# Performance work log

Hardware: AMD Instinct MI355X
Metric: run time of the kernel (lower is better)

The kernel has to match this reference:

```python
import jax, jax.numpy as jnp
import numpy as np

ALPHA = 2.0


def _masked_logsumexp(S):
    # log-sum-exp over axis 1 with the diagonal excluded (j != i)
    n = S.shape[0]
    Sm = jnp.where(jnp.eye(n, dtype=bool), -jnp.inf, S)
    return jax.nn.logsumexp(Sm, axis=1)


def setup_inputs() -> dict:
    key = jax.random.key(0)
    k1, k2, k3 = jax.random.split(key, 3)
    n, d = 8192, 128
    scale = 0.1  # keep exp(dot) in a reasonable range
    z_au = jax.random.normal(k1, (n, d), dtype=jnp.float32) * scale
    z_tp = jax.random.normal(k2, (n, d), dtype=jnp.float32) * scale
    fc_weights = jax.random.normal(k3, (2, d), dtype=jnp.float32) * scale
    return {"z_au": z_au, "z_tp": z_tp, "fc_weights": fc_weights}


def reference(z_au, z_tp, fc_weights):
    n, d = z_au.shape
    nf = jnp.float32(n)

    # pairwise dot-product similarities (cosim is a plain dot in the original)
    S_aa = z_au @ z_au.T          # [n, n]
    S_tt = z_tp @ z_tp.T          # [n, n]
    S_at = z_au @ z_tp.T          # [n, n]

    # pos_loss[i] = log(sum_{j!=i} exp(S_aa[i,j]) + exp(S_tt[i,j]))
    # implemented as a single stable logsumexp over concatenated columns
    eye = jnp.eye(n, dtype=bool)
    S_pos = jnp.concatenate(
        [jnp.where(eye, -jnp.inf, S_aa), jnp.where(eye, -jnp.inf, S_tt)], axis=1
    )  # [n, 2n]
    pos = jax.nn.logsumexp(S_pos, axis=1)  # [n]

    # neg_loss[i] = log(sum_{j!=i} exp(S_at[i,j]))
    neg = _masked_logsumexp(S_at)  # [n]

    # alpha * cosim(z_au[i], z_tp[i])
    diag_at = jnp.diagonal(S_at)  # [n]

    # supcon_loss in the original is an [n, d] tensor filled with the scalar
    # sum_i (-pos_i + neg_i + alpha * diag_i); track the scalar, account for
    # the final torch.sum over [n, d] with a factor n*d.
    supcon = jnp.sum(-pos + neg + ALPHA * diag_at)

    # pt_loss: sum_i [-<z_au_i, pt0> + <z_au_i, pt1> - <z_tp_i, pt1> + <z_tp_i, pt0>] / n
    pt0, pt1 = fc_weights[0], fc_weights[1]
    pt_loss = (
        jnp.dot(jnp.sum(z_au, axis=0), pt1 - pt0)
        + jnp.dot(jnp.sum(z_tp, axis=0), pt0 - pt1)
    ) / nf

    # esupcon_loss = 1/(n+2) * (pt_loss + supcon_loss) broadcast to [n, d];
    # torch.sum over that tensor -> multiply scalar by n*d
    return (nf * jnp.float32(d)) / (nf + 2.0) * (pt_loss + supcon)
```

## Files before the change

### kernel.cpp

```cpp
#include <hip/hip_runtime.h>

typedef __attribute__((ext_vector_type(8))) short bf16x8;
typedef __attribute__((ext_vector_type(4))) float f32x4;
typedef unsigned int u32;
typedef unsigned short u16;

#define NROWS 8192
#define NDIM 128
#define NSPLIT 16
#define COLS_PER_SPLIT (NROWS / NSPLIT)
#define BN 64
#define ITERS (COLS_PER_SPLIT / BN)

#define SQRT_LOG2E 1.2011224087864498f
#define TWO_OVER_LOG2E 1.3862943611198906f

__device__ __forceinline__ float hw_exp2(float x) {
  float r;
  asm("v_exp_f32 %0, %1" : "=v"(r) : "v"(x));
  return r;
}


__device__ __forceinline__ u16 f2bf(float x) {
  u32 u = __float_as_uint(x);
  u32 r = (u + 0x7fffu + ((u >> 16) & 1u)) >> 16;
  return (u16)r;
}

__global__ __launch_bounds__(256) void esupcon_convert(
    const float* __restrict__ za, const float* __restrict__ zt,
    const float* __restrict__ w, u16* __restrict__ zabf,
    u16* __restrict__ ztbf, float* __restrict__ pt_part) {
  const int b = blockIdx.x, t = threadIdx.x;
  const bool tp = b >= 1024;
  const float* src = tp ? zt : za;
  u16* dst = tp ? ztbf : zabf;
  const int base = ((b & 1023) * 256 + t) * 4;
  float4 v = *reinterpret_cast<const float4*>(src + base);

  const int k = base & (NDIM - 1);
  float p = v.x * (w[NDIM + k + 0] - w[k + 0]) + v.y * (w[NDIM + k + 1] - w[k + 1]) +
            v.z * (w[NDIM + k + 2] - w[k + 2]) + v.w * (w[NDIM + k + 3] - w[k + 3]);
  if (tp) p = -p;

  ushort4 o;
  o.x = f2bf(v.x * SQRT_LOG2E);
  o.y = f2bf(v.y * SQRT_LOG2E);
  o.z = f2bf(v.z * SQRT_LOG2E);
  o.w = f2bf(v.w * SQRT_LOG2E);
  *reinterpret_cast<ushort4*>(dst + base) = o;

  __shared__ float red[256];
  red[t] = p;
  __syncthreads();
  for (int st = 128; st > 0; st >>= 1) {
    if (t < st) red[t] += red[t + st];
    __syncthreads();
  }
  if (t == 0) pt_part[b] = red[0];
}


template <bool MASK>
__device__ __forceinline__ void epilogue(const f32x4 (&acc)[3][2][2],
                                         float (&poss)[2][4], float (&negs)[2][4],
                                         float* __restrict__ diagv, int wrow0,
                                         int colw0, int lane) {
#pragma unroll
  for (int rt = 0; rt < 2; ++rt)
#pragma unroll
    for (int ct = 0; ct < 2; ++ct) {
      const int col_g = colw0 + ct * 16 + (lane & 15);
      const int rbase = wrow0 + rt * 16 + ((lane >> 4) << 2);
#pragma unroll
      for (int r = 0; r < 4; ++r) {
        float eaa = hw_exp2(acc[0][rt][ct][r]);
        float ett = hw_exp2(acc[1][rt][ct][r]);
        float vat = acc[2][rt][ct][r];
        float eat = hw_exp2(vat);
        float ppos = eaa + ett;
        if (MASK) {
          const bool dia = (rbase + r) == col_g;
          if (dia) {
            diagv[rbase + r] = vat;
            ppos = 0.f;
            eat = 0.f;
          }
        }
        poss[rt][r] += ppos;
        negs[rt][r] += eat;
      }
    }
}

__global__ __launch_bounds__(256, 2) void esupcon_stage1(
    const u16* __restrict__ zabf, const u16* __restrict__ ztbf,
    float* __restrict__ pos_part, float* __restrict__ neg_part,
    float* __restrict__ diagv) {
  __shared__ __align__(16) char lds[2][32768];

  const int tid = threadIdx.x;
  const int lane = tid & 63;
  const int wid = tid >> 6;
  const int wr = wid >> 1, wc = wid & 1;
  const int by = blockIdx.x;
  const int bx = blockIdx.y;
  const int wrow0 = by * 64 + wr * 32;

  bf16x8 afrag[2][2][4];
  {
    const int rlo = lane & 15, kg = lane >> 4;
#pragma unroll
    for (int rt = 0; rt < 2; ++rt) {
      const u16* pa = zabf + (size_t)(wrow0 + rt * 16 + rlo) * NDIM + kg * 8;
      const u16* pt = ztbf + (size_t)(wrow0 + rt * 16 + rlo) * NDIM + kg * 8;
#pragma unroll
      for (int s = 0; s < 4; ++s) {
        afrag[0][rt][s] = *reinterpret_cast<const bf16x8*>(pa + s * 32);
        afrag[1][rt][s] = *reinterpret_cast<const bf16x8*>(pt + s * 32);
      }
    }
  }

  float poss[2][4], negs[2][4];
#pragma unroll
  for (int rt = 0; rt < 2; ++rt)
#pragma unroll
    for (int r = 0; r < 4; ++r) {
      poss[rt][r] = 0.f;
      negs[rt][r] = 0.f;
    }

  auto stage = [&](int buf, int it) {
    const int col0g = bx * COLS_PER_SPLIT + it * BN;
    const char* gA = (const char*)(zabf + (size_t)col0g * NDIM);
    const char* gT = (const char*)(ztbf + (size_t)col0g * NDIM);
    char* lA = &lds[buf][0];
    char* lT = &lds[buf][16384];
#pragma unroll
    for (int i = 0; i < 4; ++i) {
      const int chunk = wid * 4 + i;
      const int y = chunk * 1024 + lane * 16;
      const int ysw = y ^ (((y >> 8) & 7) << 4);
      __builtin_amdgcn_global_load_lds(
          (const __attribute__((address_space(1))) u32*)(gA + ysw),
          (__attribute__((address_space(3))) u32*)(lA + chunk * 1024), 16, 0, 0);
      __builtin_amdgcn_global_load_lds(
          (const __attribute__((address_space(1))) u32*)(gT + ysw),
          (__attribute__((address_space(3))) u32*)(lT + chunk * 1024), 16, 0, 0);
    }
  };

  int cur = 0;
  stage(0, 0);

  for (int it = 0; it < ITERS; ++it) {
    asm volatile("s_waitcnt vmcnt(0)" ::: "memory");
    __builtin_amdgcn_s_barrier();
    asm volatile("" ::: "memory");

    if (it + 1 < ITERS) stage(cur ^ 1, it + 1);

    const char* lA = &lds[cur][0];
    const char* lT = &lds[cur][16384];

    f32x4 acc[3][2][2] = {};
#pragma unroll
    for (int s = 0; s < 4; ++s) {
      bf16x8 bA[2], bT[2];
#pragma unroll
      for (int ct = 0; ct < 2; ++ct) {
        const int c = wc * 32 + ct * 16 + (lane & 15);
        const int off = (c * 256 + s * 64 + (lane >> 4) * 16) ^ ((c & 7) << 4);
        bA[ct] = *reinterpret_cast<const bf16x8*>(lA + off);
        bT[ct] = *reinterpret_cast<const bf16x8*>(lT + off);
      }
#pragma unroll
      for (int rt = 0; rt < 2; ++rt)
#pragma unroll
        for (int ct = 0; ct < 2; ++ct) {
          acc[0][rt][ct] = __builtin_amdgcn_mfma_f32_16x16x32_bf16(
              afrag[0][rt][s], bA[ct], acc[0][rt][ct], 0, 0, 0);
          acc[1][rt][ct] = __builtin_amdgcn_mfma_f32_16x16x32_bf16(
              afrag[1][rt][s], bT[ct], acc[1][rt][ct], 0, 0, 0);
          acc[2][rt][ct] = __builtin_amdgcn_mfma_f32_16x16x32_bf16(
              afrag[0][rt][s], bT[ct], acc[2][rt][ct], 0, 0, 0);
        }
    }

    const int col0g = bx * COLS_PER_SPLIT + it * BN;
    const bool hasdiag = (col0g == by * 64);
    if (hasdiag)
      epilogue<true>(acc, poss, negs, diagv, wrow0, col0g + wc * 32, lane);
    else
      epilogue<false>(acc, poss, negs, diagv, wrow0, col0g + wc * 32, lane);

    cur ^= 1;
  }

#pragma unroll
  for (int m = 1; m < 16; m <<= 1) {
#pragma unroll
    for (int rt = 0; rt < 2; ++rt)
#pragma unroll
      for (int r = 0; r < 4; ++r) {
        poss[rt][r] += __shfl_xor(poss[rt][r], m, 64);
        negs[rt][r] += __shfl_xor(negs[rt][r], m, 64);
      }
  }

  if ((lane & 15) == 0) {
    const int sp = bx * 2 + wc;
#pragma unroll
    for (int rt = 0; rt < 2; ++rt) {
      const int rbase = wrow0 + rt * 16 + ((lane >> 4) << 2);
#pragma unroll
      for (int r = 0; r < 4; ++r) {
        pos_part[(size_t)(rbase + r) * 32 + sp] = poss[rt][r];
        neg_part[(size_t)(rbase + r) * 32 + sp] = negs[rt][r];
      }
    }
  }
}


__global__ __launch_bounds__(256) void esupcon_reduce1(
    const float* __restrict__ pos_part, const float* __restrict__ neg_part,
    const float* __restrict__ diagv, const float* __restrict__ pt_part,
    float* __restrict__ part_out ) {
  const int b = blockIdx.x, t = threadIdx.x;
  const int r = b * 256 + t;
  const f32x4* pp = reinterpret_cast<const f32x4*>(pos_part + (size_t)r * 32);
  const f32x4* np = reinterpret_cast<const f32x4*>(neg_part + (size_t)r * 32);
  float P = 0.f, Nn = 0.f;
#pragma unroll
  for (int s = 0; s < 8; ++s) {
    f32x4 a = pp[s], c = np[s];
    P += a[0] + a[1] + a[2] + a[3];
    Nn += c[0] + c[1] + c[2] + c[3];
  }
  float sc = -logf(P) + logf(Nn) + TWO_OVER_LOG2E * diagv[r];
  float pt = (t < 64) ? pt_part[b * 64 + t] : 0.f;

  __shared__ float s1[256], s2[256];
  s1[t] = sc;
  s2[t] = pt;
  __syncthreads();
  for (int st = 128; st > 0; st >>= 1) {
    if (t < st) {
      s1[t] += s1[t + st];
      s2[t] += s2[t + st];
    }
    __syncthreads();
  }
  if (t == 0) {
    part_out[b] = s1[0];
    part_out[32 + b] = s2[0];
  }
}


__global__ __launch_bounds__(64) void esupcon_reduce2(
    const float* __restrict__ part_out, float* __restrict__ out) {
  const int t = threadIdx.x;
  float sc = (t < 32) ? part_out[t] : 0.f;
  float pt = (t < 32) ? part_out[32 + t] : 0.f;
#pragma unroll
  for (int m = 1; m < 64; m <<= 1) {
    sc += __shfl_xor(sc, m, 64);
    pt += __shfl_xor(pt, m, 64);
  }
  if (t == 0) {
    const float pt_loss = pt / (float)NROWS;
    out[0] = ((float)NROWS * (float)NDIM / ((float)NROWS + 2.0f)) * (pt_loss + sc);
  }
}


extern "C" void kernel_launch(void* const* d_in, const int* in_sizes, int n_in,
                              void* d_out, int out_size, void* d_ws, size_t ws_size,
                              hipStream_t stream) {
  const float* za = (const float*)d_in[0];
  const float* zt = (const float*)d_in[1];
  const float* w = (const float*)d_in[2];
  float* out = (float*)d_out;

  char* ws = (char*)d_ws;
  u16* zabf = (u16*)ws;
  u16* ztbf = (u16*)(ws + (size_t)(1 << 21));
  float* pos_part = (float*)(ws + (size_t)(2 << 21));
  float* neg_part = (float*)(ws + (size_t)(2 << 21) + (1 << 20));
  float* diagv = (float*)(ws + (size_t)(2 << 21) + (2 << 20));
  float* pt_part = (float*)(ws + (size_t)(2 << 21) + (2 << 20) + (1 << 15));
  float* part_out = (float*)(ws + (size_t)(2 << 21) + (2 << 20) + (1 << 15) + (1 << 13));

  esupcon_convert<<<dim3(2048), dim3(256), 0, stream>>>(za, zt, w, zabf, ztbf, pt_part);
  esupcon_stage1<<<dim3(NROWS / 64, NSPLIT), dim3(256), 0, stream>>>(
      zabf, ztbf, pos_part, neg_part, diagv);
  esupcon_reduce1<<<dim3(32), dim3(256), 0, stream>>>(pos_part, neg_part, diagv,
                                                      pt_part, part_out);
  esupcon_reduce2<<<dim3(1), dim3(64), 0, stream>>>(part_out, out);
}
```

Measured before the change: 80.09 us.

## Restructure stage1 into single-wave blocks with 64-row A fragments and 16-column tiles

Each block becomes one 64-lane wavefront that keeps A and T fragments for 64 rows in registers and streams 16-column tiles of both matrices through double-buffered LDS. Waiting on vmcnt(8) after issuing the next tile's loads replaces the block-wide barrier, so the next prefetch overlaps the current tile's compute. The goal is to drop the cross-wave barrier and raise B-operand reuse per LDS load across four row tiles. In exchange, register pressure goes up and grid parallelism per block goes down. The partial layout shrinks to 16 strips per row, and reduce1 is updated to match.

```diff
diff --git a/kernel.cpp b/kernel.cpp
--- a/kernel.cpp
+++ b/kernel.cpp
@@ -7,10 +7,10 @@
 
 #define NROWS 8192
 #define NDIM 128
-#define NSPLIT 16
-#define COLS_PER_SPLIT (NROWS / NSPLIT)
-#define BN 64
-#define ITERS (COLS_PER_SPLIT / BN)
+#define NSTRIP 16
+#define COLS_PER_STRIP (NROWS / NSTRIP)
+#define BN 16
+#define WITERS (COLS_PER_STRIP / BN)
 
 #define SQRT_LOG2E 1.2011224087864498f
 #define TWO_OVER_LOG2E 1.3862943611198906f
@@ -63,146 +63,140 @@
 
 
 template <bool MASK>
-__device__ __forceinline__ void epilogue(const f32x4 (&acc)[3][2][2],
-                                         float (&poss)[2][4], float (&negs)[2][4],
-                                         float* __restrict__ diagv, int wrow0,
-                                         int colw0, int lane) {
-#pragma unroll
-  for (int rt = 0; rt < 2; ++rt)
-#pragma unroll
-    for (int ct = 0; ct < 2; ++ct) {
-      const int col_g = colw0 + ct * 16 + (lane & 15);
-      const int rbase = wrow0 + rt * 16 + ((lane >> 4) << 2);
-#pragma unroll
-      for (int r = 0; r < 4; ++r) {
-        float eaa = hw_exp2(acc[0][rt][ct][r]);
-        float ett = hw_exp2(acc[1][rt][ct][r]);
-        float vat = acc[2][rt][ct][r];
-        float eat = hw_exp2(vat);
-        float ppos = eaa + ett;
-        if (MASK) {
-          const bool dia = (rbase + r) == col_g;
-          if (dia) {
-            diagv[rbase + r] = vat;
-            ppos = 0.f;
-            eat = 0.f;
-          }
+__device__ __forceinline__ void compute_tile(
+    const char* __restrict__ lA, const char* __restrict__ lT,
+    const bf16x8 (&afA)[4][4], const bf16x8 (&afT)[4][4],
+    float (&poss)[4][4], float (&negs)[4][4], float* __restrict__ diagv,
+    int row0, int col0, int lane) {
+  const int lc = lane & 15, kg = lane >> 4;
+  const int colg = col0 + lc;
+
+  f32x4 accA[4] = {};
+#pragma unroll
+  for (int s = 0; s < 4; ++s) {
+    const int off = (lc * 256 + s * 64 + kg * 16) ^ ((lc & 7) << 4);
+    bf16x8 b = *reinterpret_cast<const bf16x8*>(lA + off);
+#pragma unroll
+    for (int rt = 0; rt < 4; ++rt)
+      accA[rt] = __builtin_amdgcn_mfma_f32_16x16x32_bf16(afA[rt][s], b, accA[rt], 0, 0, 0);
+  }
+#pragma unroll
+  for (int rt = 0; rt < 4; ++rt)
+#pragma unroll
+    for (int r = 0; r < 4; ++r) {
+      float e = hw_exp2(accA[rt][r]);
+      if (MASK && (row0 + rt * 16 + kg * 4 + r) == colg) e = 0.f;
+      poss[rt][r] += e;
+    }
+
+  f32x4 accT[4] = {}, accX[4] = {};
+#pragma unroll
+  for (int s = 0; s < 4; ++s) {
+    const int off = (lc * 256 + s * 64 + kg * 16) ^ ((lc & 7) << 4);
+    bf16x8 b = *reinterpret_cast<const bf16x8*>(lT + off);
+#pragma unroll
+    for (int rt = 0; rt < 4; ++rt) {
+      accT[rt] = __builtin_amdgcn_mfma_f32_16x16x32_bf16(afT[rt][s], b, accT[rt], 0, 0, 0);
+      accX[rt] = __builtin_amdgcn_mfma_f32_16x16x32_bf16(afA[rt][s], b, accX[rt], 0, 0, 0);
+    }
+  }
+#pragma unroll
+  for (int rt = 0; rt < 4; ++rt)
+#pragma unroll
+    for (int r = 0; r < 4; ++r) {
+      float ett = hw_exp2(accT[rt][r]);
+      float vat = accX[rt][r];
+      float eat = hw_exp2(vat);
+      if (MASK) {
+        const bool dia = (row0 + rt * 16 + kg * 4 + r) == colg;
+        if (dia) {
+          diagv[colg] = vat;
+          ett = 0.f;
+          eat = 0.f;
         }
-        poss[rt][r] += ppos;
-        negs[rt][r] += eat;
-      }
-    }
-}
-
-__global__ __launch_bounds__(256, 2) void esupcon_stage1(
+      }
+      poss[rt][r] += ett;
+      negs[rt][r] += eat;
+    }
+}
+
+__global__ __launch_bounds__(64, 2) void esupcon_stage1(
     const u16* __restrict__ zabf, const u16* __restrict__ ztbf,
     float* __restrict__ pos_part, float* __restrict__ neg_part,
     float* __restrict__ diagv) {
-  __shared__ __align__(16) char lds[2][32768];
-
-  const int tid = threadIdx.x;
-  const int lane = tid & 63;
-  const int wid = tid >> 6;
-  const int wr = wid >> 1, wc = wid & 1;
-  const int by = blockIdx.x;
-  const int bx = blockIdx.y;
-  const int wrow0 = by * 64 + wr * 32;
-
-  bf16x8 afrag[2][2][4];
+  __shared__ __align__(16) char lds[2][8192];
+
+  const int lane = threadIdx.x;
+  const int rg = blockIdx.x;
+  const int cs = blockIdx.y;
+  const int row0 = rg * 64;
+
+  bf16x8 afA[4][4], afT[4][4];
   {
     const int rlo = lane & 15, kg = lane >> 4;
 #pragma unroll
-    for (int rt = 0; rt < 2; ++rt) {
-      const u16* pa = zabf + (size_t)(wrow0 + rt * 16 + rlo) * NDIM + kg * 8;
-      const u16* pt = ztbf + (size_t)(wrow0 + rt * 16 + rlo) * NDIM + kg * 8;
+    for (int rt = 0; rt < 4; ++rt) {
+      const u16* pa = zabf + (size_t)(row0 + rt * 16 + rlo) * NDIM + kg * 8;
+      const u16* pt = ztbf + (size_t)(row0 + rt * 16 + rlo) * NDIM + kg * 8;
 #pragma unroll
       for (int s = 0; s < 4; ++s) {
-        afrag[0][rt][s] = *reinterpret_cast<const bf16x8*>(pa + s * 32);
-        afrag[1][rt][s] = *reinterpret_cast<const bf16x8*>(pt + s * 32);
-      }
-    }
-  }
-
-  float poss[2][4], negs[2][4];
-#pragma unroll
-  for (int rt = 0; rt < 2; ++rt)
-#pragma unroll
-    for (int r = 0; r < 4; ++r) {
-      poss[rt][r] = 0.f;
-      negs[rt][r] = 0.f;
-    }
+        afA[rt][s] = *reinterpret_cast<const bf16x8*>(pa + s * 32);
+        afT[rt][s] = *reinterpret_cast<const bf16x8*>(pt + s * 32);
+      }
+    }
+  }
+
+  float poss[4][4] = {}, negs[4][4] = {};
 
   auto stage = [&](int buf, int it) {
-    const int col0g = bx * COLS_PER_SPLIT + it * BN;
-    const char* gA = (const char*)(zabf + (size_t)col0g * NDIM);
-    const char* gT = (const char*)(ztbf + (size_t)col0g * NDIM);
-    char* lA = &lds[buf][0];
-    char* lT = &lds[buf][16384];
-#pragma unroll
-    for (int i = 0; i < 4; ++i) {
-      const int chunk = wid * 4 + i;
-      const int y = chunk * 1024 + lane * 16;
+    const size_t colbase = (size_t)(cs * COLS_PER_STRIP + it * BN) * NDIM;
+    const char* gA = (const char*)(zabf + colbase);
+    const char* gT = (const char*)(ztbf + colbase);
+    char* dst = &lds[buf][0];
+#pragma unroll
+    for (int j = 0; j < 4; ++j) {
+      const int y = j * 1024 + lane * 16;
       const int ysw = y ^ (((y >> 8) & 7) << 4);
       __builtin_amdgcn_global_load_lds(
           (const __attribute__((address_space(1))) u32*)(gA + ysw),
-          (__attribute__((address_space(3))) u32*)(lA + chunk * 1024), 16, 0, 0);
+          (__attribute__((address_space(3))) u32*)(dst + j * 1024), 16, 0, 0);
+    }
+#pragma unroll
+    for (int j = 0; j < 4; ++j) {
+      const int y = j * 1024 + lane * 16;
+      const int ysw = y ^ (((y >> 8) & 7) << 4);
       __builtin_amdgcn_global_load_lds(
           (const __attribute__((address_space(1))) u32*)(gT + ysw),
-          (__attribute__((address_space(3))) u32*)(lT + chunk * 1024), 16, 0, 0);
+          (__attribute__((address_space(3))) u32*)(dst + 4096 + j * 1024), 16, 0, 0);
     }
   };
 
+  stage(0, 0);
   int cur = 0;
-  stage(0, 0);
-
-  for (int it = 0; it < ITERS; ++it) {
-    asm volatile("s_waitcnt vmcnt(0)" ::: "memory");
-    __builtin_amdgcn_s_barrier();
-    asm volatile("" ::: "memory");
-
-    if (it + 1 < ITERS) stage(cur ^ 1, it + 1);
-
-    const char* lA = &lds[cur][0];
-    const char* lT = &lds[cur][16384];
-
-    f32x4 acc[3][2][2] = {};
-#pragma unroll
-    for (int s = 0; s < 4; ++s) {
-      bf16x8 bA[2], bT[2];
-#pragma unroll
-      for (int ct = 0; ct < 2; ++ct) {
-        const int c = wc * 32 + ct * 16 + (lane & 15);
-        const int off = (c * 256 + s * 64 + (lane >> 4) * 16) ^ ((c & 7) << 4);
-        bA[ct] = *reinterpret_cast<const bf16x8*>(lA + off);
-        bT[ct] = *reinterpret_cast<const bf16x8*>(lT + off);
-      }
-#pragma unroll
-      for (int rt = 0; rt < 2; ++rt)
-#pragma unroll
-        for (int ct = 0; ct < 2; ++ct) {
-          acc[0][rt][ct] = __builtin_amdgcn_mfma_f32_16x16x32_bf16(
-              afrag[0][rt][s], bA[ct], acc[0][rt][ct], 0, 0, 0);
-          acc[1][rt][ct] = __builtin_amdgcn_mfma_f32_16x16x32_bf16(
-              afrag[1][rt][s], bT[ct], acc[1][rt][ct], 0, 0, 0);
-          acc[2][rt][ct] = __builtin_amdgcn_mfma_f32_16x16x32_bf16(
-              afrag[0][rt][s], bT[ct], acc[2][rt][ct], 0, 0, 0);
-        }
-    }
-
-    const int col0g = bx * COLS_PER_SPLIT + it * BN;
-    const bool hasdiag = (col0g == by * 64);
+  for (int it = 0; it < WITERS; ++it) {
+    if (it + 1 < WITERS) {
+      stage(cur ^ 1, it + 1);
+      asm volatile("s_waitcnt vmcnt(8)" ::: "memory");
+    } else {
+      asm volatile("s_waitcnt vmcnt(0)" ::: "memory");
+    }
+    __builtin_amdgcn_sched_barrier(0);
+
+    const int col0 = cs * COLS_PER_STRIP + it * BN;
+    const bool hasdiag = ((col0 >> 6) == rg);
     if (hasdiag)
-      epilogue<true>(acc, poss, negs, diagv, wrow0, col0g + wc * 32, lane);
+      compute_tile<true>(&lds[cur][0], &lds[cur][4096], afA, afT, poss, negs,
+                         diagv, row0, col0, lane);
     else
-      epilogue<false>(acc, poss, negs, diagv, wrow0, col0g + wc * 32, lane);
-
+      compute_tile<false>(&lds[cur][0], &lds[cur][4096], afA, afT, poss, negs,
+                          diagv, row0, col0, lane);
     cur ^= 1;
   }
 
 #pragma unroll
   for (int m = 1; m < 16; m <<= 1) {
 #pragma unroll
-    for (int rt = 0; rt < 2; ++rt)
+    for (int rt = 0; rt < 4; ++rt)
 #pragma unroll
       for (int r = 0; r < 4; ++r) {
         poss[rt][r] += __shfl_xor(poss[rt][r], m, 64);
@@ -211,16 +205,15 @@
   }
 
   if ((lane & 15) == 0) {
-    const int sp = bx * 2 + wc;
-#pragma unroll
-    for (int rt = 0; rt < 2; ++rt) {
-      const int rbase = wrow0 + rt * 16 + ((lane >> 4) << 2);
+    const int kg = lane >> 4;
+#pragma unroll
+    for (int rt = 0; rt < 4; ++rt)
 #pragma unroll
       for (int r = 0; r < 4; ++r) {
-        pos_part[(size_t)(rbase + r) * 32 + sp] = poss[rt][r];
-        neg_part[(size_t)(rbase + r) * 32 + sp] = negs[rt][r];
-      }
-    }
+        const int row = row0 + rt * 16 + kg * 4 + r;
+        pos_part[(size_t)row * NSTRIP + cs] = poss[rt][r];
+        neg_part[(size_t)row * NSTRIP + cs] = negs[rt][r];
+      }
   }
 }
 
@@ -231,11 +224,11 @@
     float* __restrict__ part_out ) {
   const int b = blockIdx.x, t = threadIdx.x;
   const int r = b * 256 + t;
-  const f32x4* pp = reinterpret_cast<const f32x4*>(pos_part + (size_t)r * 32);
-  const f32x4* np = reinterpret_cast<const f32x4*>(neg_part + (size_t)r * 32);
+  const f32x4* pp = reinterpret_cast<const f32x4*>(pos_part + (size_t)r * NSTRIP);
+  const f32x4* np = reinterpret_cast<const f32x4*>(neg_part + (size_t)r * NSTRIP);
   float P = 0.f, Nn = 0.f;
 #pragma unroll
-  for (int s = 0; s < 8; ++s) {
+  for (int s = 0; s < 4; ++s) {
     f32x4 a = pp[s], c = np[s];
     P += a[0] + a[1] + a[2] + a[3];
     Nn += c[0] + c[1] + c[2] + c[3];
@@ -296,7 +289,7 @@
   float* part_out = (float*)(ws + (size_t)(2 << 21) + (2 << 20) + (1 << 15) + (1 << 13));
 
   esupcon_convert<<<dim3(2048), dim3(256), 0, stream>>>(za, zt, w, zabf, ztbf, pt_part);
-  esupcon_stage1<<<dim3(NROWS / 64, NSPLIT), dim3(256), 0, stream>>>(
+  esupcon_stage1<<<dim3(NROWS / 64, NSTRIP), dim3(64), 0, stream>>>(
       zabf, ztbf, pos_part, neg_part, diagv);
   esupcon_reduce1<<<dim3(32), dim3(256), 0, stream>>>(pos_part, neg_part, diagv,
                                                       pt_part, part_out);
```

After: 84.72 us. 5.8% more time.
